# Performance work log

Hardware: AMD Instinct MI355X
Metric: run time of the kernel (lower is better)

The kernel has to match this reference:

```python
import jax, jax.numpy as jnp
import numpy as np

N_QUBITS = 8
N_LAYERS = 4
BATCH = 4096


def _ry(theta):
    # RY(theta) = [[cos(t/2), -sin(t/2)], [sin(t/2), cos(t/2)]]
    c = jnp.cos(theta / 2).astype(jnp.complex64)
    s = jnp.sin(theta / 2).astype(jnp.complex64)
    return jnp.stack([jnp.stack([c, -s], axis=-1),
                      jnp.stack([s, c], axis=-1)], axis=-2)  # (..., 2, 2)


def _rz(theta):
    # RZ(theta) = diag(exp(-i t/2), exp(+i t/2))
    p = jnp.exp(-0.5j * theta.astype(jnp.complex64))
    z = jnp.zeros_like(p)
    return jnp.stack([jnp.stack([p, z], axis=-1),
                      jnp.stack([z, jnp.conj(p)], axis=-1)], axis=-2)


def _apply_1q(state, U, w):
    # state: (B, 2, 2, ..., 2); apply 2x2 unitary U on wire w (axis 1+w).
    st = jnp.moveaxis(state, 1 + w, -1)
    if U.ndim == 3:  # per-sample (batched) gate, U: (B, 2, 2)
        st = jnp.einsum('bij,b...j->b...i', U, st)
    else:            # shared gate, U: (2, 2)
        st = jnp.einsum('ij,b...j->b...i', U, st)
    return jnp.moveaxis(st, -1, 1 + w)


def _apply_cnot(state, c, t):
    # flip target wire t where control wire c is |1>
    st = jnp.moveaxis(state, (1 + c, 1 + t), (-2, -1))
    st = jnp.concatenate([st[..., 0:1, :], st[..., 1:2, ::-1]], axis=-2)
    return jnp.moveaxis(st, (-2, -1), (1 + c, 1 + t))


def _circuit(x, weights):
    B = x.shape[0]
    state = jnp.zeros((B,) + (2,) * N_QUBITS, jnp.complex64)
    state = state.at[(slice(None),) + (0,) * N_QUBITS].set(1.0)  # |0...0>
    # Angle encoding: RY(x_i) on each wire, batched over samples
    for i in range(N_QUBITS):
        state = _apply_1q(state, _ry(x[:, i]), i)
    # Variational layers: CNOT ring then RY/RZ rotations
    for l in range(N_LAYERS):
        for i in range(N_QUBITS):
            state = _apply_cnot(state, i, (i + 1) % N_QUBITS)
        for i in range(N_QUBITS):
            state = _apply_1q(state, _ry(weights[l, i, 0]), i)
            state = _apply_1q(state, _rz(weights[l, i, 1]), i)
    # <Z_0> = P(q0=0) - P(q0=1)
    probs = jnp.sum(jnp.abs(state.reshape(B, 2, -1)) ** 2, axis=-1)
    return (probs[:, 0] - probs[:, 1]).astype(jnp.float32)


def setup_inputs() -> dict:
    key = jax.random.key(0)
    k1, k2 = jax.random.split(key)
    x = jax.random.uniform(k1, (BATCH, N_QUBITS), dtype=jnp.float32) * jnp.pi
    weights = jax.random.normal(k2, (N_LAYERS, N_QUBITS, 2), dtype=jnp.float32) * 0.1
    return {"x": x, "weights": weights}


def reference(x, weights):
    return _circuit(x, weights)
```

## Files before the change

kernel.cpp:

```cpp
#include <hip/hip_runtime.h>

#define NQ 8
#define NL 4
#define BATCH 4096


template <int CTRL>
__device__ __forceinline__ float dppx(float v) {
  return __int_as_float(
      __builtin_amdgcn_update_dpp(0, __float_as_int(v), CTRL, 0xF, 0xF, true));
}

__device__ __forceinline__ float swz4(float v) {
  return __int_as_float(
      __builtin_amdgcn_ds_swizzle(__float_as_int(v), 0x101F));
}

template <int W>
__device__ __forceinline__ float xl(float v) {
  if constexpr (W == 0) return dppx<0x128>(v);
  else if constexpr (W == 1) return swz4(v);
  else if constexpr (W == 2) return dppx<0x4E>(v);
  else return dppx<0xB1>(v);
}

template <int W>
__device__ __forceinline__ void ry_gate(float re[16], float im[16],
                                        float c, float s, int lane) {
  if constexpr (W <= 3) {
    const float ss = ((lane >> (3 - W)) & 1) ? s : -s;
#pragma unroll
    for (int r = 0; r < 16; ++r) {
      float pr = xl<W>(re[r]);
      float pi = xl<W>(im[r]);
      re[r] = c * re[r] + ss * pr;
      im[r] = c * im[r] + ss * pi;
    }
  } else {
    constexpr int m = 1 << (7 - W);
#pragma unroll
    for (int r = 0; r < 16; ++r) {
      if ((r & m) == 0) {
        const int r1 = r | m;
        float a0r = re[r], a1r = re[r1];
        float a0i = im[r], a1i = im[r1];
        re[r]  = c * a0r - s * a1r;
        re[r1] = s * a0r + c * a1r;
        im[r]  = c * a0i - s * a1i;
        im[r1] = s * a0i + c * a1i;
      }
    }
  }
}

template <int W>
__device__ __forceinline__ void rz_gate(float re[16], float im[16],
                                        float c, float s, int lane) {
  if constexpr (W <= 3) {
    const float ss = ((lane >> (3 - W)) & 1) ? s : -s;
#pragma unroll
    for (int r = 0; r < 16; ++r) {
      float nr = re[r] * c - im[r] * ss;
      float ni = im[r] * c + re[r] * ss;
      re[r] = nr; im[r] = ni;
    }
  } else {
    constexpr int m = 1 << (7 - W);
#pragma unroll
    for (int r = 0; r < 16; ++r) {
      const float ss = (r & m) ? s : -s;
      float nr = re[r] * c - im[r] * ss;
      float ni = im[r] * c + re[r] * ss;
      re[r] = nr; im[r] = ni;
    }
  }
}

__device__ __forceinline__ void cnot_ring(float re[16], float im[16], int lane) {
  {
    const bool p = (lane & 8) != 0;
#pragma unroll
    for (int r = 0; r < 16; ++r) {
      float pr = swz4(re[r]), pi = swz4(im[r]);
      re[r] = p ? pr : re[r];
      im[r] = p ? pi : im[r];
    }
  }
  {
    const bool p = (lane & 4) != 0;
#pragma unroll
    for (int r = 0; r < 16; ++r) {
      float pr = dppx<0x4E>(re[r]), pi = dppx<0x4E>(im[r]);
      re[r] = p ? pr : re[r];
      im[r] = p ? pi : im[r];
    }
  }
  {
    const bool p = (lane & 2) != 0;
#pragma unroll
    for (int r = 0; r < 16; ++r) {
      float pr = dppx<0xB1>(re[r]), pi = dppx<0xB1>(im[r]);
      re[r] = p ? pr : re[r];
      im[r] = p ? pi : im[r];
    }
  }
  {
    const bool p = (lane & 1) != 0;
#pragma unroll
    for (int r = 0; r < 8; ++r) {
      float t0r = re[r], t1r = re[r + 8];
      re[r] = p ? t1r : t0r; re[r + 8] = p ? t0r : t1r;
      float t0i = im[r], t1i = im[r + 8];
      im[r] = p ? t1i : t0i; im[r + 8] = p ? t0i : t1i;
    }
  }
#pragma unroll
  for (int r = 8; r < 12; ++r) {
    float t = re[r]; re[r] = re[r + 4]; re[r + 4] = t;
    t = im[r]; im[r] = im[r + 4]; im[r + 4] = t;
  }
#pragma unroll
  for (int r = 0; r < 16; ++r) {
    if ((r & 4) && !(r & 2)) {
      float t = re[r]; re[r] = re[r | 2]; re[r | 2] = t;
      t = im[r]; im[r] = im[r | 2]; im[r | 2] = t;
    }
  }
#pragma unroll
  for (int r = 0; r < 16; ++r) {
    if ((r & 2) && !(r & 1)) {
      float t = re[r]; re[r] = re[r | 1]; re[r | 1] = t;
      t = im[r]; im[r] = im[r | 1]; im[r | 1] = t;
    }
  }
#pragma unroll
  for (int r = 1; r < 16; r += 2) {
    re[r] = dppx<0x128>(re[r]);
    im[r] = dppx<0x128>(im[r]);
  }
}

__global__ __launch_bounds__(256) void vqc_kernel(const float* __restrict__ x,
                                                  const float* __restrict__ w,
                                                  float* __restrict__ out) {
  const int lane = (int)(threadIdx.x & 63);
  const int wv = (int)((blockIdx.x * blockDim.x + threadIdx.x) >> 6);
  const int s = wv * 4 + (lane >> 4);

  float re[16], im[16];
#pragma unroll
  for (int r = 0; r < 16; ++r) { re[r] = 0.f; im[r] = 0.f; }
  if ((lane & 15) == 0) re[0] = 1.f;

  {
    const float4 x0 = *(const float4*)&x[s * 8];
    const float4 x1 = *(const float4*)&x[s * 8 + 4];
    float c, sn;
    __sincosf(x0.x * 0.5f, &sn, &c); ry_gate<0>(re, im, c, sn, lane);
    __sincosf(x0.y * 0.5f, &sn, &c); ry_gate<1>(re, im, c, sn, lane);
    __sincosf(x0.z * 0.5f, &sn, &c); ry_gate<2>(re, im, c, sn, lane);
    __sincosf(x0.w * 0.5f, &sn, &c); ry_gate<3>(re, im, c, sn, lane);
    __sincosf(x1.x * 0.5f, &sn, &c); ry_gate<4>(re, im, c, sn, lane);
    __sincosf(x1.y * 0.5f, &sn, &c); ry_gate<5>(re, im, c, sn, lane);
    __sincosf(x1.z * 0.5f, &sn, &c); ry_gate<6>(re, im, c, sn, lane);
    __sincosf(x1.w * 0.5f, &sn, &c); ry_gate<7>(re, im, c, sn, lane);
  }

#pragma unroll
  for (int l = 0; l < NL; ++l) {
    cnot_ring(re, im, lane);
    const float* wl = &w[l * NQ * 2];
#define APPLY_ROT(W) { float cy, sy, cz, sz;            \
    __sincosf(wl[(W) * 2 + 0] * 0.5f, &sy, &cy);        \
    __sincosf(wl[(W) * 2 + 1] * 0.5f, &sz, &cz);        \
    ry_gate<W>(re, im, cy, sy, lane);                   \
    rz_gate<W>(re, im, cz, sz, lane); }
    APPLY_ROT(0) APPLY_ROT(1) APPLY_ROT(2) APPLY_ROT(3)
    APPLY_ROT(4) APPLY_ROT(5) APPLY_ROT(6) APPLY_ROT(7)
#undef APPLY_ROT
  }

  float acc = 0.f;
#pragma unroll
  for (int r = 0; r < 16; ++r) acc += re[r] * re[r] + im[r] * im[r];
  acc = (lane & 8) ? -acc : acc;
  acc += dppx<0xB1>(acc);
  acc += dppx<0x4E>(acc);
  acc += swz4(acc);
  acc += dppx<0x128>(acc);
  if ((lane & 15) == 0) out[s] = acc;
}

extern "C" void kernel_launch(void* const* d_in, const int* in_sizes, int n_in,
                              void* d_out, int out_size, void* d_ws, size_t ws_size,
                              hipStream_t stream) {
  const float* x = (const float*)d_in[0];
  const float* w = (const float*)d_in[1];
  float* out = (float*)d_out;
  (void)in_sizes; (void)n_in; (void)out_size; (void)d_ws; (void)ws_size;

  dim3 grid(BATCH / 16), block(256);
  hipLaunchKernelGGL(vqc_kernel, grid, block, 0, stream, x, w, out);
}
```

Before: 65.81 us.

## Map one sample per wavefront with 4 amplitudes per lane and bpermute CNOT ring

Changes the decomposition from 16 lanes per sample holding 16 amplitudes each to a full 64-lane wavefront per sample holding 4 amplitudes per lane. The CNOT ring becomes a single Gray-code permutation done with ds_bpermute plus register selects. Rotations in the final layer that cannot affect <Z_0> are dropped, leaving only RY on wire 0. The intent is to cut register pressure and per-lane serial work and to raise wave count, at the cost of four times more waves and LDS-path bpermute traffic.

New measurement: 63.90 us. -2.9%, faster.

```diff
diff --git a/kernel.cpp b/kernel.cpp
--- a/kernel.cpp
+++ b/kernel.cpp
@@ -11,35 +11,42 @@
       __builtin_amdgcn_update_dpp(0, __float_as_int(v), CTRL, 0xF, 0xF, true));
 }
 
+__device__ __forceinline__ float swz16(float v) {
+  return __int_as_float(__builtin_amdgcn_ds_swizzle(__float_as_int(v), 0x401F));
+}
 __device__ __forceinline__ float swz4(float v) {
-  return __int_as_float(
-      __builtin_amdgcn_ds_swizzle(__float_as_int(v), 0x101F));
+  return __int_as_float(__builtin_amdgcn_ds_swizzle(__float_as_int(v), 0x101F));
+}
+__device__ __forceinline__ float bperm(int addr, float v) {
+  return __int_as_float(__builtin_amdgcn_ds_bpermute(addr, __float_as_int(v)));
 }
 
 template <int W>
-__device__ __forceinline__ float xl(float v) {
-  if constexpr (W == 0) return dppx<0x128>(v);
-  else if constexpr (W == 1) return swz4(v);
-  else if constexpr (W == 2) return dppx<0x4E>(v);
+__device__ __forceinline__ float xl(float v, int bp32) {
+  if constexpr (W == 0) return bperm(bp32, v);
+  else if constexpr (W == 1) return swz16(v);
+  else if constexpr (W == 2) return dppx<0x128>(v);
+  else if constexpr (W == 3) return swz4(v);
+  else if constexpr (W == 4) return dppx<0x4E>(v);
   else return dppx<0xB1>(v);
 }
 
 template <int W>
-__device__ __forceinline__ void ry_gate(float re[16], float im[16],
-                                        float c, float s, int lane) {
-  if constexpr (W <= 3) {
-    const float ss = ((lane >> (3 - W)) & 1) ? s : -s;
+__device__ __forceinline__ void ry_gate(float re[4], float im[4],
+                                        float c, float s, int lane, int bp32) {
+  if constexpr (W <= 5) {
+    const float ss = ((lane >> (5 - W)) & 1) ? s : -s;
 #pragma unroll
-    for (int r = 0; r < 16; ++r) {
-      float pr = xl<W>(re[r]);
-      float pi = xl<W>(im[r]);
+    for (int r = 0; r < 4; ++r) {
+      float pr = xl<W>(re[r], bp32);
+      float pi = xl<W>(im[r], bp32);
       re[r] = c * re[r] + ss * pr;
       im[r] = c * im[r] + ss * pi;
     }
   } else {
     constexpr int m = 1 << (7 - W);
 #pragma unroll
-    for (int r = 0; r < 16; ++r) {
+    for (int r = 0; r < 4; ++r) {
       if ((r & m) == 0) {
         const int r1 = r | m;
         float a0r = re[r], a1r = re[r1];
@@ -54,12 +61,12 @@
 }
 
 template <int W>
-__device__ __forceinline__ void rz_gate(float re[16], float im[16],
+__device__ __forceinline__ void rz_gate(float re[4], float im[4],
                                         float c, float s, int lane) {
-  if constexpr (W <= 3) {
-    const float ss = ((lane >> (3 - W)) & 1) ? s : -s;
+  if constexpr (W <= 5) {
+    const float ss = ((lane >> (5 - W)) & 1) ? s : -s;
 #pragma unroll
-    for (int r = 0; r < 16; ++r) {
+    for (int r = 0; r < 4; ++r) {
       float nr = re[r] * c - im[r] * ss;
       float ni = im[r] * c + re[r] * ss;
       re[r] = nr; im[r] = ni;
@@ -67,7 +74,7 @@
   } else {
     constexpr int m = 1 << (7 - W);
 #pragma unroll
-    for (int r = 0; r < 16; ++r) {
+    for (int r = 0; r < 4; ++r) {
       const float ss = (r & m) ? s : -s;
       float nr = re[r] * c - im[r] * ss;
       float ni = im[r] * c + re[r] * ss;
@@ -76,119 +83,88 @@
   }
 }
 
-__device__ __forceinline__ void cnot_ring(float re[16], float im[16], int lane) {
-  {
-    const bool p = (lane & 8) != 0;
-#pragma unroll
-    for (int r = 0; r < 16; ++r) {
-      float pr = swz4(re[r]), pi = swz4(im[r]);
-      re[r] = p ? pr : re[r];
-      im[r] = p ? pi : im[r];
-    }
-  }
-  {
-    const bool p = (lane & 4) != 0;
-#pragma unroll
-    for (int r = 0; r < 16; ++r) {
-      float pr = dppx<0x4E>(re[r]), pi = dppx<0x4E>(im[r]);
-      re[r] = p ? pr : re[r];
-      im[r] = p ? pi : im[r];
-    }
-  }
-  {
-    const bool p = (lane & 2) != 0;
-#pragma unroll
-    for (int r = 0; r < 16; ++r) {
-      float pr = dppx<0xB1>(re[r]), pi = dppx<0xB1>(im[r]);
-      re[r] = p ? pr : re[r];
-      im[r] = p ? pi : im[r];
-    }
-  }
-  {
-    const bool p = (lane & 1) != 0;
-#pragma unroll
-    for (int r = 0; r < 8; ++r) {
-      float t0r = re[r], t1r = re[r + 8];
-      re[r] = p ? t1r : t0r; re[r + 8] = p ? t0r : t1r;
-      float t0i = im[r], t1i = im[r + 8];
-      im[r] = p ? t1i : t0i; im[r + 8] = p ? t0i : t1i;
-    }
-  }
-#pragma unroll
-  for (int r = 8; r < 12; ++r) {
-    float t = re[r]; re[r] = re[r + 4]; re[r + 4] = t;
-    t = im[r]; im[r] = im[r + 4]; im[r + 4] = t;
-  }
-#pragma unroll
-  for (int r = 0; r < 16; ++r) {
-    if ((r & 4) && !(r & 2)) {
-      float t = re[r]; re[r] = re[r | 2]; re[r | 2] = t;
-      t = im[r]; im[r] = im[r | 2]; im[r | 2] = t;
-    }
-  }
-#pragma unroll
-  for (int r = 0; r < 16; ++r) {
-    if ((r & 2) && !(r & 1)) {
-      float t = re[r]; re[r] = re[r | 1]; re[r | 1] = t;
-      t = im[r]; im[r] = im[r | 1]; im[r | 1] = t;
-    }
-  }
-#pragma unroll
-  for (int r = 1; r < 16; r += 2) {
-    re[r] = dppx<0x128>(re[r]);
-    im[r] = dppx<0x128>(im[r]);
-  }
+__device__ __forceinline__ void ring(float re[4], float im[4],
+                                     int addr_e, int addr_o, bool p2) {
+  const float t0r = p2 ? re[2] : re[0];
+  const float t1r = p2 ? re[3] : re[1];
+  const float t2r = p2 ? re[1] : re[3];
+  const float t3r = p2 ? re[0] : re[2];
+  const float t0i = p2 ? im[2] : im[0];
+  const float t1i = p2 ? im[3] : im[1];
+  const float t2i = p2 ? im[1] : im[3];
+  const float t3i = p2 ? im[0] : im[2];
+  re[0] = bperm(addr_e, t0r);
+  re[1] = bperm(addr_o, t1r);
+  re[2] = bperm(addr_e, t2r);
+  re[3] = bperm(addr_o, t3r);
+  im[0] = bperm(addr_e, t0i);
+  im[1] = bperm(addr_o, t1i);
+  im[2] = bperm(addr_e, t2i);
+  im[3] = bperm(addr_o, t3i);
 }
 
-__global__ __launch_bounds__(256) void vqc_kernel(const float* __restrict__ x,
-                                                  const float* __restrict__ w,
-                                                  float* __restrict__ out) {
+__global__ __launch_bounds__(256, 4) void vqc_kernel(const float* __restrict__ x,
+                                                     const float* __restrict__ w,
+                                                     float* __restrict__ out) {
   const int lane = (int)(threadIdx.x & 63);
-  const int wv = (int)((blockIdx.x * blockDim.x + threadIdx.x) >> 6);
-  const int s = wv * 4 + (lane >> 4);
+  const int s = (int)((blockIdx.x * blockDim.x + threadIdx.x) >> 6);
 
-  float re[16], im[16];
-#pragma unroll
-  for (int r = 0; r < 16; ++r) { re[r] = 0.f; im[r] = 0.f; }
-  if ((lane & 15) == 0) re[0] = 1.f;
+  const int gray   = lane ^ (lane >> 1);
+  const int addr_e = gray << 2;
+  const int addr_o = addr_e ^ 0xC0;
+  const bool p2    = (__popc(lane) & 1) != 0;
+  const int bp32   = (lane ^ 32) << 2;
+
+  float re[4] = {0.f, 0.f, 0.f, 0.f};
+  float im[4] = {0.f, 0.f, 0.f, 0.f};
+  if (lane == 0) re[0] = 1.f;
 
   {
     const float4 x0 = *(const float4*)&x[s * 8];
     const float4 x1 = *(const float4*)&x[s * 8 + 4];
     float c, sn;
-    __sincosf(x0.x * 0.5f, &sn, &c); ry_gate<0>(re, im, c, sn, lane);
-    __sincosf(x0.y * 0.5f, &sn, &c); ry_gate<1>(re, im, c, sn, lane);
-    __sincosf(x0.z * 0.5f, &sn, &c); ry_gate<2>(re, im, c, sn, lane);
-    __sincosf(x0.w * 0.5f, &sn, &c); ry_gate<3>(re, im, c, sn, lane);
-    __sincosf(x1.x * 0.5f, &sn, &c); ry_gate<4>(re, im, c, sn, lane);
-    __sincosf(x1.y * 0.5f, &sn, &c); ry_gate<5>(re, im, c, sn, lane);
-    __sincosf(x1.z * 0.5f, &sn, &c); ry_gate<6>(re, im, c, sn, lane);
-    __sincosf(x1.w * 0.5f, &sn, &c); ry_gate<7>(re, im, c, sn, lane);
+    __sincosf(x0.x * 0.5f, &sn, &c); ry_gate<0>(re, im, c, sn, lane, bp32);
+    __sincosf(x0.y * 0.5f, &sn, &c); ry_gate<1>(re, im, c, sn, lane, bp32);
+    __sincosf(x0.z * 0.5f, &sn, &c); ry_gate<2>(re, im, c, sn, lane, bp32);
+    __sincosf(x0.w * 0.5f, &sn, &c); ry_gate<3>(re, im, c, sn, lane, bp32);
+    __sincosf(x1.x * 0.5f, &sn, &c); ry_gate<4>(re, im, c, sn, lane, bp32);
+    __sincosf(x1.y * 0.5f, &sn, &c); ry_gate<5>(re, im, c, sn, lane, bp32);
+    __sincosf(x1.z * 0.5f, &sn, &c); ry_gate<6>(re, im, c, sn, lane, bp32);
+    __sincosf(x1.w * 0.5f, &sn, &c); ry_gate<7>(re, im, c, sn, lane, bp32);
   }
 
 #pragma unroll
-  for (int l = 0; l < NL; ++l) {
-    cnot_ring(re, im, lane);
+  for (int l = 0; l < NL - 1; ++l) {
+    ring(re, im, addr_e, addr_o, p2);
     const float* wl = &w[l * NQ * 2];
 #define APPLY_ROT(W) { float cy, sy, cz, sz;            \
     __sincosf(wl[(W) * 2 + 0] * 0.5f, &sy, &cy);        \
     __sincosf(wl[(W) * 2 + 1] * 0.5f, &sz, &cz);        \
-    ry_gate<W>(re, im, cy, sy, lane);                   \
+    ry_gate<W>(re, im, cy, sy, lane, bp32);             \
     rz_gate<W>(re, im, cz, sz, lane); }
     APPLY_ROT(0) APPLY_ROT(1) APPLY_ROT(2) APPLY_ROT(3)
     APPLY_ROT(4) APPLY_ROT(5) APPLY_ROT(6) APPLY_ROT(7)
 #undef APPLY_ROT
   }
 
+  ring(re, im, addr_e, addr_o, p2);
+  {
+    float cy, sy;
+    __sincosf(w[(NL - 1) * NQ * 2 + 0] * 0.5f, &sy, &cy);
+    ry_gate<0>(re, im, cy, sy, lane, bp32);
+  }
+
   float acc = 0.f;
 #pragma unroll
-  for (int r = 0; r < 16; ++r) acc += re[r] * re[r] + im[r] * im[r];
-  acc = (lane & 8) ? -acc : acc;
+  for (int r = 0; r < 4; ++r) acc += re[r] * re[r] + im[r] * im[r];
+  acc = (lane & 32) ? -acc : acc;
   acc += dppx<0xB1>(acc);
   acc += dppx<0x4E>(acc);
   acc += swz4(acc);
   acc += dppx<0x128>(acc);
-  if ((lane & 15) == 0) out[s] = acc;
+  acc += swz16(acc);
+  acc += bperm(bp32, acc);
+  if (lane == 0) out[s] = acc;
 }
 
 extern "C" void kernel_launch(void* const* d_in, const int* in_sizes, int n_in,
@@ -199,6 +175,6 @@
   float* out = (float*)d_out;
   (void)in_sizes; (void)n_in; (void)out_size; (void)d_ws; (void)ws_size;
 
-  dim3 grid(BATCH / 16), block(256);
+  dim3 grid(BATCH * 64 / 256), block(256);
   hipLaunchKernelGGL(vqc_kernel, grid, block, 0, stream, x, w, out);
 }
```
